# Performance work log

Hardware: AMD Instinct MI355X
Metric: run time of the kernel (lower is better)

## Reference

```python
import jax, jax.numpy as jnp
import numpy as np

NUM_HEADS = 16
D_KV = 64
NUM_BUCKETS = 32
MAX_DISTANCE = 128


def _relative_position_bucket(rel_pos, num_buckets=NUM_BUCKETS, max_distance=MAX_DISTANCE):
    # bidirectional bucketing (dec_or_not=False -> b_di=True in source)
    nb = num_buckets // 2
    buckets = (rel_pos > 0).astype(jnp.int32) * nb
    rel = jnp.abs(rel_pos)
    max_exact = nb // 2
    is_small = rel < max_exact
    # guard log(0); masked out by is_small anyway
    rel_if_large = max_exact + (
        jnp.log(jnp.maximum(rel, 1).astype(jnp.float32) / max_exact)
        / np.log(max_distance / max_exact) * (nb - max_exact)
    ).astype(jnp.int32)
    rel_if_large = jnp.minimum(rel_if_large, nb - 1)
    return buckets + jnp.where(is_small, rel, rel_if_large)


def setup_inputs() -> dict:
    key = jax.random.key(0)
    ks = jax.random.split(key, 6)
    B, S, D = 2, 2048, 1024
    s = 1.0 / np.sqrt(D)
    return {
        "hidden_states": jax.random.normal(ks[0], (B, S, D), jnp.float32),
        "Wq": jax.random.normal(ks[1], (D, NUM_HEADS * D_KV), jnp.float32) * s,
        "Wk": jax.random.normal(ks[2], (D, NUM_HEADS * D_KV), jnp.float32) * s,
        "Wv": jax.random.normal(ks[3], (D, NUM_HEADS * D_KV), jnp.float32) * s,
        "Wo": jax.random.normal(ks[4], (NUM_HEADS * D_KV, D), jnp.float32) * s,
        "rel_emb": jax.random.normal(ks[5], (NUM_BUCKETS, NUM_HEADS), jnp.float32),
    }


def reference(hidden_states, Wq, Wk, Wv, Wo, rel_emb):
    B, S, D = hidden_states.shape
    H, Dh = NUM_HEADS, D_KV

    def heads(x):  # [B,S,H*Dh] -> [B,H,S,Dh]
        return x.reshape(B, S, H, Dh).transpose(0, 2, 1, 3)

    q = heads(hidden_states @ Wq)
    k = heads(hidden_states @ Wk)
    v = heads(hidden_states @ Wv)

    # T5 attention: no 1/sqrt(d) scaling
    scores = jnp.einsum("bhqd,bhkd->bhqk", q, k)

    # relative position bias (bias_cal)
    pos = jnp.arange(S)
    rel_pos = pos[None, :] - pos[:, None]  # [S_q, S_k]
    buckets = _relative_position_bucket(rel_pos)
    bias = rel_emb[buckets]                       # [S,S,H]
    bias = bias.transpose(2, 0, 1)[None]          # [1,H,S,S]

    scores = scores + bias
    attn = jax.nn.softmax(scores.astype(jnp.float32), axis=-1).astype(scores.dtype)
    # dropout p=0 in eval -> identity
    out = jnp.einsum("bhqk,bhkd->bhqd", attn, v)
    out = out.transpose(0, 2, 1, 3).reshape(B, S, H * Dh)
    return out @ Wo
```

## Files before the change

kernel.cpp:

```cpp
#include <hip/hip_runtime.h>

typedef __bf16 bf16x8 __attribute__((ext_vector_type(8)));
typedef float f32x4 __attribute__((ext_vector_type(4)));

#define LDK 72
#define LOG2E 1.44269504088896f

__device__ __forceinline__ unsigned short bfbits(float x) {
  __bf16 h = (__bf16)x;
  return __builtin_bit_cast(unsigned short, h);
}

__device__ __forceinline__ void gload_lds16(const unsigned short* g, unsigned short* l) {
  __builtin_amdgcn_global_load_lds(
      (const __attribute__((address_space(1))) unsigned int*)(const void*)g,
      (__attribute__((address_space(3))) unsigned int*)(void*)l, 16, 0, 0);
}

__global__ void bias_table_kernel(const float* __restrict__ rel_emb,
                                  float* __restrict__ tab) {
  int i = blockIdx.x * 256 + threadIdx.x;
  int h = i >> 12;
  int idx = i & 4095;
  int rp = idx - 2048;
  int base = (rp > 0) ? 16 : 0;
  int rel = rp < 0 ? -rp : rp;
  int b;
  if (rel < 8) {
    b = rel;
  } else {
    b = 8 + (int)(log2f((float)rel * 0.125f) * 2.0f);
    if (b > 15) b = 15;
  }
  tab[h * 4096 + idx] = rel_emb[(base + b) * 16 + h] * LOG2E - 64.0f;
}

__global__ __launch_bounds__(256)
void hid_convert_kernel(const float* __restrict__ src, unsigned short* __restrict__ dst) {
  int idx = (blockIdx.x * 256 + threadIdx.x) * 8;
  float4 v0 = *(const float4*)(src + idx);
  float4 v1 = *(const float4*)(src + idx + 4);
  unsigned short o[8] = {bfbits(v0.x), bfbits(v0.y), bfbits(v0.z), bfbits(v0.w),
                         bfbits(v1.x), bfbits(v1.y), bfbits(v1.z), bfbits(v1.w)};
  *(uint4*)(dst + idx) = *(const uint4*)o;
}

__global__ __launch_bounds__(256)
void transpose_w_kernel(const float* __restrict__ W0, const float* __restrict__ W1,
                        const float* __restrict__ W2, const float* __restrict__ W3,
                        unsigned short* __restrict__ T0, unsigned short* __restrict__ T1,
                        unsigned short* __restrict__ T2, unsigned short* __restrict__ T3) {
  __shared__ __align__(16) unsigned short Tlds[64 * 68];
  const int mz = blockIdx.z;
  const float* W = mz == 0 ? W0 : (mz == 1 ? W1 : (mz == 2 ? W2 : W3));
  unsigned short* T = mz == 0 ? T0 : (mz == 1 ? T1 : (mz == 2 ? T2 : T3));
  const int k0 = blockIdx.y * 64, n0 = blockIdx.x * 64, tid = threadIdx.x;
#pragma unroll
  for (int p = 0; p < 4; ++p) {
    int idx = p * 256 + tid;
    int kk = idx >> 4, nc = idx & 15;
    float4 v = *(const float4*)(W + (size_t)(k0 + kk) * 1024 + n0 + nc * 4);
    ushort4 s;
    s.x = bfbits(v.x); s.y = bfbits(v.y); s.z = bfbits(v.z); s.w = bfbits(v.w);
    *(ushort4*)(Tlds + kk * 68 + nc * 4) = s;
  }
  __syncthreads();
#pragma unroll
  for (int p = 0; p < 2; ++p) {
    int idx = p * 256 + tid;
    int n = idx >> 3, c = idx & 7;
    unsigned short tmp[8];
#pragma unroll
    for (int j = 0; j < 8; ++j) tmp[j] = Tlds[(c * 8 + j) * 68 + n];
    *(uint4*)(T + (size_t)(n0 + n) * 1024 + k0 + c * 8) = *(const uint4*)tmp;
  }
}

template <bool OUT_F32, int BN>
__global__ __launch_bounds__(256)
void gemm_kernel(const unsigned short* __restrict__ A,
                 const unsigned short* __restrict__ Wt0,
                 const unsigned short* __restrict__ Wt1,
                 const unsigned short* __restrict__ Wt2,
                 void* __restrict__ O0v, void* __restrict__ O1v, void* __restrict__ O2v,
                 float scale0) {
  constexpr int NBLK = 1024 / BN;
  constexpr int NT = BN / 32;
  __shared__ __align__(16) unsigned short Alds[128 * 64];
  __shared__ __align__(16) unsigned short Wlds[BN * 64];
  const int tid = threadIdx.x;
  const int which = blockIdx.x / NBLK;
  const int n0 = (blockIdx.x % NBLK) * BN;
  const int m0 = blockIdx.y * 128;
  const unsigned short* Wt = which == 0 ? Wt0 : (which == 1 ? Wt1 : Wt2);
  void* Ov = which == 0 ? O0v : (which == 1 ? O1v : O2v);
  const int wave = tid >> 6, lane = tid & 63, quad = lane >> 4, col = lane & 15;
  const int wm = (wave >> 1) * 64, wn = (wave & 1) * (BN / 2);
  const int wbase = tid & ~63;
  const int sw = col & 7;

  f32x4 acc[4][NT] = {};

  for (int kt = 0; kt < 16; ++kt) {
    const int k0 = kt * 64;
    __syncthreads();
#pragma unroll
    for (int p = 0; p < 4; ++p) {
      int idx = p * 256 + tid;
      int m = idx >> 3, c = idx & 7;
      int cs = c ^ (m & 7);
      gload_lds16(A + (size_t)(m0 + m) * 1024 + k0 + cs * 8,
                  Alds + (size_t)(p * 256 + wbase) * 8);
    }
#pragma unroll
    for (int p = 0; p < BN / 32; ++p) {
      int idx = p * 256 + tid;
      int n = idx >> 3, c = idx & 7;
      int cs = c ^ (n & 7);
      gload_lds16(Wt + (size_t)(n0 + n) * 1024 + k0 + cs * 8,
                  Wlds + (size_t)(p * 256 + wbase) * 8);
    }
    __syncthreads();
#pragma unroll
    for (int ks = 0; ks < 2; ++ks) {
      bf16x8 af[4], wf[NT];
      const int j = ((ks * 4) ^ sw) ^ (sw & 3);
#pragma unroll
      for (int mt = 0; mt < 4; ++mt)
        af[mt] = *(const bf16x8*)(Alds + (wm + mt * 16 + col) * 64 +
                                  (((ks * 4 + quad) ^ sw) * 8));
#pragma unroll
      for (int nt = 0; nt < NT; ++nt)
        wf[nt] = *(const bf16x8*)(Wlds + (wn + nt * 16 + col) * 64 +
                                  (((ks * 4 + quad) ^ sw) * 8));
      (void)j;
#pragma unroll
      for (int mt = 0; mt < 4; ++mt)
#pragma unroll
        for (int nt = 0; nt < NT; ++nt)
          acc[mt][nt] = __builtin_amdgcn_mfma_f32_16x16x32_bf16(af[mt], wf[nt], acc[mt][nt], 0, 0, 0);
    }
  }
  if (!OUT_F32 && which == 2) {
    unsigned short* Ot = (unsigned short*)Ov;
#pragma unroll
    for (int nt = 0; nt < NT; ++nt)
#pragma unroll
      for (int mt = 0; mt < 4; ++mt) {
        int n = n0 + wn + nt * 16 + col;
        int m = m0 + wm + mt * 16 + quad * 4;
        ushort4 s;
        s.x = bfbits(acc[mt][nt][0]); s.y = bfbits(acc[mt][nt][1]);
        s.z = bfbits(acc[mt][nt][2]); s.w = bfbits(acc[mt][nt][3]);
        *(ushort4*)(Ot + (size_t)n * 4096 + m) = s;
      }
  } else {
    const float sc = (which == 0) ? scale0 : 1.0f;
#pragma unroll
    for (int mt = 0; mt < 4; ++mt)
#pragma unroll
      for (int nt = 0; nt < NT; ++nt)
#pragma unroll
        for (int r = 0; r < 4; ++r) {
          int m = m0 + wm + mt * 16 + quad * 4 + r;
          int n = n0 + wn + nt * 16 + col;
          float x = acc[mt][nt][r] * sc;
          if (OUT_F32)
            ((float*)Ov)[(size_t)m * 1024 + n] = x;
          else
            ((unsigned short*)Ov)[(size_t)m * 1024 + n] = bfbits(x);
        }
  }
}

__global__ __launch_bounds__(256)
void attn_kernel(unsigned short* __restrict__ q_ws,
                 const unsigned short* __restrict__ k_ws,
                 const unsigned short* __restrict__ vt_ws,
                 const float* __restrict__ bias_tab) {
  __shared__ __align__(16) unsigned short Klds[64 * 64];
  __shared__ __align__(16) unsigned short Vlds[64 * 64];
  __shared__ __align__(16) unsigned short Plds[128 * LDK];
  __shared__ float bias_lds[192];
  __shared__ float l_sh[128];
  const int tid = threadIdx.x;
  const int q0 = blockIdx.x * 128;
  const int bh = blockIdx.y;
  const int b = bh >> 4, h = bh & 15;
  const int wave = tid >> 6, lane = tid & 63, quad = lane >> 4, col = lane & 15;
  const int wbase = tid & ~63;
  const int sw = col & 7;

  bf16x8 qf[2][2];
#pragma unroll
  for (int nt = 0; nt < 2; ++nt) {
    size_t row = (size_t)(b * 2048 + q0 + wave * 32 + nt * 16 + col) * 1024 + h * 64;
    qf[nt][0] = *(const bf16x8*)(q_ws + row + quad * 8);
    qf[nt][1] = *(const bf16x8*)(q_ws + row + 32 + quad * 8);
  }
  const float bias_far_pos = bias_tab[h * 4096 + 2048 + 512];
  const float bias_far_neg = bias_tab[h * 4096 + 2048 - 512];

  float l_lane[2] = {0.f, 0.f};
  f32x4 of[2][4] = {};

  for (int kt = 0; kt < 32; ++kt) {
    const int k0 = kt * 64;
    const int diff = k0 - q0;
    const bool far = (diff >= 256) || (diff <= -192);
    __syncthreads();
#pragma unroll
    for (int p = 0; p < 2; ++p) {
      int idx = p * 256 + tid;
      int key = idx >> 3, c = idx & 7;
      int cs = c ^ (key & 7);
      gload_lds16(k_ws + (size_t)(b * 2048 + k0 + key) * 1024 + h * 64 + cs * 8,
                  Klds + (size_t)(p * 256 + wbase) * 8);
    }
#pragma unroll
    for (int p = 0; p < 2; ++p) {
      int idx = p * 256 + tid;
      int d = idx >> 3, c = idx & 7;
      int cs = c ^ (d & 7);
      gload_lds16(vt_ws + (size_t)(h * 64 + d) * 4096 + b * 2048 + k0 + cs * 8,
                  Vlds + (size_t)(p * 256 + wbase) * 8);
    }
    if (!far && tid < 191)
      bias_lds[tid] = bias_tab[h * 4096 + 2048 + k0 - q0 - 127 + tid];
    __syncthreads();

    f32x4 st[4][2];
    if (far) {
      const float c0 = (diff > 0) ? bias_far_pos : bias_far_neg;
#pragma unroll
      for (int mt = 0; mt < 4; ++mt)
#pragma unroll
        for (int nt = 0; nt < 2; ++nt)
#pragma unroll
          for (int r = 0; r < 4; ++r) st[mt][nt][r] = c0;
    } else {
#pragma unroll
      for (int mt = 0; mt < 4; ++mt)
#pragma unroll
        for (int nt = 0; nt < 2; ++nt)
#pragma unroll
          for (int r = 0; r < 4; ++r)
            st[mt][nt][r] =
                bias_lds[(mt * 16 + quad * 4 + r) - (wave * 32 + nt * 16 + col) + 127];
    }
#pragma unroll
    for (int ks = 0; ks < 2; ++ks)
#pragma unroll
      for (int mt = 0; mt < 4; ++mt) {
        bf16x8 kf = *(const bf16x8*)(Klds + (mt * 16 + col) * 64 +
                                     (((ks * 4 + quad) ^ sw) * 8));
        st[mt][0] = __builtin_amdgcn_mfma_f32_16x16x32_bf16(kf, qf[0][ks], st[mt][0], 0, 0, 0);
        st[mt][1] = __builtin_amdgcn_mfma_f32_16x16x32_bf16(kf, qf[1][ks], st[mt][1], 0, 0, 0);
      }

#pragma unroll
    for (int nt = 0; nt < 2; ++nt)
#pragma unroll
      for (int mt = 0; mt < 4; ++mt) {
        float p0 = __builtin_amdgcn_exp2f(st[mt][nt][0]);
        float p1 = __builtin_amdgcn_exp2f(st[mt][nt][1]);
        float p2 = __builtin_amdgcn_exp2f(st[mt][nt][2]);
        float p3 = __builtin_amdgcn_exp2f(st[mt][nt][3]);
        l_lane[nt] += (p0 + p1) + (p2 + p3);
        ushort4 pk;
        pk.x = bfbits(p0); pk.y = bfbits(p1); pk.z = bfbits(p2); pk.w = bfbits(p3);
        *(ushort4*)(Plds + (wave * 32 + nt * 16 + col) * LDK + mt * 16 + quad * 4) = pk;
      }
    __threadfence_block();

#pragma unroll
    for (int ks = 0; ks < 2; ++ks) {
      bf16x8 pf0 = *(const bf16x8*)(Plds + (wave * 32 + col) * LDK + ks * 32 + quad * 8);
      bf16x8 pf1 = *(const bf16x8*)(Plds + (wave * 32 + 16 + col) * LDK + ks * 32 + quad * 8);
#pragma unroll
      for (int dn = 0; dn < 4; ++dn) {
        bf16x8 vf = *(const bf16x8*)(Vlds + (dn * 16 + col) * 64 +
                                     (((ks * 4 + quad) ^ sw) * 8));
        of[0][dn] = __builtin_amdgcn_mfma_f32_16x16x32_bf16(pf0, vf, of[0][dn], 0, 0, 0);
        of[1][dn] = __builtin_amdgcn_mfma_f32_16x16x32_bf16(pf1, vf, of[1][dn], 0, 0, 0);
      }
    }
  }

#pragma unroll
  for (int nt = 0; nt < 2; ++nt) {
    l_lane[nt] += __shfl_xor(l_lane[nt], 16, 64);
    l_lane[nt] += __shfl_xor(l_lane[nt], 32, 64);
  }
  l_sh[wave * 32 + col] = l_lane[0];
  l_sh[wave * 32 + 16 + col] = l_lane[1];
  __syncthreads();
#pragma unroll
  for (int mtp = 0; mtp < 2; ++mtp)
#pragma unroll
    for (int r = 0; r < 4; ++r) {
      float inv = 1.0f / fmaxf(l_sh[wave * 32 + mtp * 16 + quad * 4 + r], 1e-30f);
      size_t row = (size_t)(b * 2048 + q0 + wave * 32 + mtp * 16 + quad * 4 + r);
#pragma unroll
      for (int dn = 0; dn < 4; ++dn)
        q_ws[row * 1024 + h * 64 + dn * 16 + col] = bfbits(of[mtp][dn][r] * inv);
    }
}

extern "C" void kernel_launch(void* const* d_in, const int* in_sizes, int n_in,
                              void* d_out, int out_size, void* d_ws, size_t ws_size,
                              hipStream_t stream) {
  const float* hidden = (const float*)d_in[0];
  const float* Wq = (const float*)d_in[1];
  const float* Wk = (const float*)d_in[2];
  const float* Wv = (const float*)d_in[3];
  const float* Wo = (const float*)d_in[4];
  const float* rel_emb = (const float*)d_in[5];
  float* out = (float*)d_out;

  unsigned short* q_ws = (unsigned short*)d_ws;
  unsigned short* k_ws = q_ws + 4194304;
  unsigned short* vt_ws = k_ws + 4194304;
  unsigned short* wt_q = vt_ws + 4194304;
  unsigned short* wt_k = wt_q + 1048576;
  unsigned short* wt_v = wt_k + 1048576;
  unsigned short* wt_o = wt_v + 1048576;
  float* bias_tab = (float*)(wt_o + 1048576);
  unsigned short* hid_bf = (unsigned short*)d_out;

  bias_table_kernel<<<256, 256, 0, stream>>>(rel_emb, bias_tab);
  hid_convert_kernel<<<2048, 256, 0, stream>>>(hidden, hid_bf);
  transpose_w_kernel<<<dim3(16, 16, 4), 256, 0, stream>>>(
      Wq, Wk, Wv, Wo, wt_q, wt_k, wt_v, wt_o);
  gemm_kernel<false, 128><<<dim3(24, 32), 256, 0, stream>>>(
      hid_bf, wt_q, wt_k, wt_v, q_ws, k_ws, vt_ws, LOG2E);
  attn_kernel<<<dim3(16, 32), 256, 0, stream>>>(q_ws, k_ws, vt_ws, bias_tab);
  gemm_kernel<true, 64><<<dim3(16, 32), 256, 0, stream>>>(
      q_ws, wt_o, wt_o, wt_o, out, out, out, 1.0f);
}
```

Baseline: 204.4 us.

## Double-buffer attention K/V/bias tiles and merge prelude kernels into one launch

The attention loop now keeps two LDS buffers for the K, V and bias tiles. It issues the asynchronous global-to-LDS loads for the next key tile right after the barrier, so they overlap the current tile's QK, exp and PV MFMA work, and one of the two barriers per iteration goes away. The bias-table, hidden-state conversion and weight-transpose kernels are merged into a single prelude launch that branches on block index, which removes two launch gaps. In exchange, LDS use per attention block roughly doubles for the K/V tiles, which could lower occupancy. The GEMM kernel also loses an unused variable.

```diff
diff --git a/kernel.cpp b/kernel.cpp
--- a/kernel.cpp
+++ b/kernel.cpp
@@ -17,62 +17,62 @@
       (__attribute__((address_space(3))) unsigned int*)(void*)l, 16, 0, 0);
 }
 
-__global__ void bias_table_kernel(const float* __restrict__ rel_emb,
-                                  float* __restrict__ tab) {
-  int i = blockIdx.x * 256 + threadIdx.x;
-  int h = i >> 12;
-  int idx = i & 4095;
-  int rp = idx - 2048;
-  int base = (rp > 0) ? 16 : 0;
-  int rel = rp < 0 ? -rp : rp;
-  int b;
-  if (rel < 8) {
-    b = rel;
+__global__ __launch_bounds__(256)
+void prelude_kernel(const float* __restrict__ hidden, unsigned short* __restrict__ hid_bf,
+                    const float* __restrict__ W0, const float* __restrict__ W1,
+                    const float* __restrict__ W2, const float* __restrict__ W3,
+                    unsigned short* __restrict__ T0, unsigned short* __restrict__ T1,
+                    unsigned short* __restrict__ T2, unsigned short* __restrict__ T3,
+                    const float* __restrict__ rel_emb, float* __restrict__ bias_tab) {
+  __shared__ __align__(16) unsigned short Tlds[64 * 68];
+  const int bx = blockIdx.x, tid = threadIdx.x;
+  if (bx < 2048) {
+    int idx = (bx * 256 + tid) * 8;
+    float4 v0 = *(const float4*)(hidden + idx);
+    float4 v1 = *(const float4*)(hidden + idx + 4);
+    unsigned short o[8] = {bfbits(v0.x), bfbits(v0.y), bfbits(v0.z), bfbits(v0.w),
+                           bfbits(v1.x), bfbits(v1.y), bfbits(v1.z), bfbits(v1.w)};
+    *(uint4*)(hid_bf + idx) = *(const uint4*)o;
+  } else if (bx < 3072) {
+    int flat = bx - 2048;
+    int mz = flat >> 8;
+    int k0 = ((flat >> 4) & 15) * 64, n0 = (flat & 15) * 64;
+    const float* W = mz == 0 ? W0 : (mz == 1 ? W1 : (mz == 2 ? W2 : W3));
+    unsigned short* T = mz == 0 ? T0 : (mz == 1 ? T1 : (mz == 2 ? T2 : T3));
+#pragma unroll
+    for (int p = 0; p < 4; ++p) {
+      int idx = p * 256 + tid;
+      int kk = idx >> 4, nc = idx & 15;
+      float4 v = *(const float4*)(W + (size_t)(k0 + kk) * 1024 + n0 + nc * 4);
+      ushort4 s;
+      s.x = bfbits(v.x); s.y = bfbits(v.y); s.z = bfbits(v.z); s.w = bfbits(v.w);
+      *(ushort4*)(Tlds + kk * 68 + nc * 4) = s;
+    }
+    __syncthreads();
+#pragma unroll
+    for (int p = 0; p < 2; ++p) {
+      int idx = p * 256 + tid;
+      int n = idx >> 3, c = idx & 7;
+      unsigned short tmp[8];
+#pragma unroll
+      for (int j = 0; j < 8; ++j) tmp[j] = Tlds[(c * 8 + j) * 68 + n];
+      *(uint4*)(T + (size_t)(n0 + n) * 1024 + k0 + c * 8) = *(const uint4*)tmp;
+    }
   } else {
-    b = 8 + (int)(log2f((float)rel * 0.125f) * 2.0f);
-    if (b > 15) b = 15;
-  }
-  tab[h * 4096 + idx] = rel_emb[(base + b) * 16 + h] * LOG2E - 64.0f;
-}
-
-__global__ __launch_bounds__(256)
-void hid_convert_kernel(const float* __restrict__ src, unsigned short* __restrict__ dst) {
-  int idx = (blockIdx.x * 256 + threadIdx.x) * 8;
-  float4 v0 = *(const float4*)(src + idx);
-  float4 v1 = *(const float4*)(src + idx + 4);
-  unsigned short o[8] = {bfbits(v0.x), bfbits(v0.y), bfbits(v0.z), bfbits(v0.w),
-                         bfbits(v1.x), bfbits(v1.y), bfbits(v1.z), bfbits(v1.w)};
-  *(uint4*)(dst + idx) = *(const uint4*)o;
-}
-
-__global__ __launch_bounds__(256)
-void transpose_w_kernel(const float* __restrict__ W0, const float* __restrict__ W1,
-                        const float* __restrict__ W2, const float* __restrict__ W3,
-                        unsigned short* __restrict__ T0, unsigned short* __restrict__ T1,
-                        unsigned short* __restrict__ T2, unsigned short* __restrict__ T3) {
-  __shared__ __align__(16) unsigned short Tlds[64 * 68];
-  const int mz = blockIdx.z;
-  const float* W = mz == 0 ? W0 : (mz == 1 ? W1 : (mz == 2 ? W2 : W3));
-  unsigned short* T = mz == 0 ? T0 : (mz == 1 ? T1 : (mz == 2 ? T2 : T3));
-  const int k0 = blockIdx.y * 64, n0 = blockIdx.x * 64, tid = threadIdx.x;
-#pragma unroll
-  for (int p = 0; p < 4; ++p) {
-    int idx = p * 256 + tid;
-    int kk = idx >> 4, nc = idx & 15;
-    float4 v = *(const float4*)(W + (size_t)(k0 + kk) * 1024 + n0 + nc * 4);
-    ushort4 s;
-    s.x = bfbits(v.x); s.y = bfbits(v.y); s.z = bfbits(v.z); s.w = bfbits(v.w);
-    *(ushort4*)(Tlds + kk * 68 + nc * 4) = s;
-  }
-  __syncthreads();
-#pragma unroll
-  for (int p = 0; p < 2; ++p) {
-    int idx = p * 256 + tid;
-    int n = idx >> 3, c = idx & 7;
-    unsigned short tmp[8];
-#pragma unroll
-    for (int j = 0; j < 8; ++j) tmp[j] = Tlds[(c * 8 + j) * 68 + n];
-    *(uint4*)(T + (size_t)(n0 + n) * 1024 + k0 + c * 8) = *(const uint4*)tmp;
+    int i = (bx - 3072) * 256 + tid;
+    int h = i >> 12;
+    int idx = i & 4095;
+    int rp = idx - 2048;
+    int base = (rp > 0) ? 16 : 0;
+    int rel = rp < 0 ? -rp : rp;
+    int b;
+    if (rel < 8) {
+      b = rel;
+    } else {
+      b = 8 + (int)(log2f((float)rel * 0.125f) * 2.0f);
+      if (b > 15) b = 15;
+    }
+    bias_tab[h * 4096 + idx] = rel_emb[(base + b) * 16 + h] * LOG2E - 64.0f;
   }
 }
 
@@ -124,7 +124,6 @@
 #pragma unroll
     for (int ks = 0; ks < 2; ++ks) {
       bf16x8 af[4], wf[NT];
-      const int j = ((ks * 4) ^ sw) ^ (sw & 3);
 #pragma unroll
       for (int mt = 0; mt < 4; ++mt)
         af[mt] = *(const bf16x8*)(Alds + (wm + mt * 16 + col) * 64 +
@@ -133,7 +132,6 @@
       for (int nt = 0; nt < NT; ++nt)
         wf[nt] = *(const bf16x8*)(Wlds + (wn + nt * 16 + col) * 64 +
                                   (((ks * 4 + quad) ^ sw) * 8));
-      (void)j;
 #pragma unroll
       for (int mt = 0; mt < 4; ++mt)
 #pragma unroll
@@ -178,10 +176,10 @@
                  const unsigned short* __restrict__ k_ws,
                  const unsigned short* __restrict__ vt_ws,
                  const float* __restrict__ bias_tab) {
-  __shared__ __align__(16) unsigned short Klds[64 * 64];
-  __shared__ __align__(16) unsigned short Vlds[64 * 64];
+  __shared__ __align__(16) unsigned short Klds[2][64 * 64];
+  __shared__ __align__(16) unsigned short Vlds[2][64 * 64];
   __shared__ __align__(16) unsigned short Plds[128 * LDK];
-  __shared__ float bias_lds[192];
+  __shared__ float bias_lds[2][192];
   __shared__ float l_sh[128];
   const int tid = threadIdx.x;
   const int q0 = blockIdx.x * 128;
@@ -204,30 +202,39 @@
   float l_lane[2] = {0.f, 0.f};
   f32x4 of[2][4] = {};
 
+  auto stage = [&](int kt, int buf) {
+    const int k0 = kt * 64;
+#pragma unroll
+    for (int p = 0; p < 2; ++p) {
+      int idx = p * 256 + tid;
+      int key = idx >> 3, c = idx & 7;
+      int cs = c ^ (key & 7);
+      gload_lds16(k_ws + (size_t)(b * 2048 + k0 + key) * 1024 + h * 64 + cs * 8,
+                  Klds[buf] + (size_t)(p * 256 + wbase) * 8);
+    }
+#pragma unroll
+    for (int p = 0; p < 2; ++p) {
+      int idx = p * 256 + tid;
+      int d = idx >> 3, c = idx & 7;
+      int cs = c ^ (d & 7);
+      gload_lds16(vt_ws + (size_t)(h * 64 + d) * 4096 + b * 2048 + k0 + cs * 8,
+                  Vlds[buf] + (size_t)(p * 256 + wbase) * 8);
+    }
+    const int diff = k0 - q0;
+    const bool farr = (diff >= 256) || (diff <= -192);
+    if (!farr && tid < 191)
+      bias_lds[buf][tid] = bias_tab[h * 4096 + 2048 + k0 - q0 - 127 + tid];
+  };
+
+  stage(0, 0);
+
   for (int kt = 0; kt < 32; ++kt) {
+    const int cur = kt & 1;
     const int k0 = kt * 64;
     const int diff = k0 - q0;
     const bool far = (diff >= 256) || (diff <= -192);
     __syncthreads();
-#pragma unroll
-    for (int p = 0; p < 2; ++p) {
-      int idx = p * 256 + tid;
-      int key = idx >> 3, c = idx & 7;
-      int cs = c ^ (key & 7);
-      gload_lds16(k_ws + (size_t)(b * 2048 + k0 + key) * 1024 + h * 64 + cs * 8,
-                  Klds + (size_t)(p * 256 + wbase) * 8);
-    }
-#pragma unroll
-    for (int p = 0; p < 2; ++p) {
-      int idx = p * 256 + tid;
-      int d = idx >> 3, c = idx & 7;
-      int cs = c ^ (d & 7);
-      gload_lds16(vt_ws + (size_t)(h * 64 + d) * 4096 + b * 2048 + k0 + cs * 8,
-                  Vlds + (size_t)(p * 256 + wbase) * 8);
-    }
-    if (!far && tid < 191)
-      bias_lds[tid] = bias_tab[h * 4096 + 2048 + k0 - q0 - 127 + tid];
-    __syncthreads();
+    if (kt + 1 < 32) stage(kt + 1, cur ^ 1);
 
     f32x4 st[4][2];
     if (far) {
@@ -246,13 +253,13 @@
 #pragma unroll
           for (int r = 0; r < 4; ++r)
             st[mt][nt][r] =
-                bias_lds[(mt * 16 + quad * 4 + r) - (wave * 32 + nt * 16 + col) + 127];
+                bias_lds[cur][(mt * 16 + quad * 4 + r) - (wave * 32 + nt * 16 + col) + 127];
     }
 #pragma unroll
     for (int ks = 0; ks < 2; ++ks)
 #pragma unroll
       for (int mt = 0; mt < 4; ++mt) {
-        bf16x8 kf = *(const bf16x8*)(Klds + (mt * 16 + col) * 64 +
+        bf16x8 kf = *(const bf16x8*)(Klds[cur] + (mt * 16 + col) * 64 +
                                      (((ks * 4 + quad) ^ sw) * 8));
         st[mt][0] = __builtin_amdgcn_mfma_f32_16x16x32_bf16(kf, qf[0][ks], st[mt][0], 0, 0, 0);
         st[mt][1] = __builtin_amdgcn_mfma_f32_16x16x32_bf16(kf, qf[1][ks], st[mt][1], 0, 0, 0);
@@ -279,7 +286,7 @@
       bf16x8 pf1 = *(const bf16x8*)(Plds + (wave * 32 + 16 + col) * LDK + ks * 32 + quad * 8);
 #pragma unroll
       for (int dn = 0; dn < 4; ++dn) {
-        bf16x8 vf = *(const bf16x8*)(Vlds + (dn * 16 + col) * 64 +
+        bf16x8 vf = *(const bf16x8*)(Vlds[cur] + (dn * 16 + col) * 64 +
                                      (((ks * 4 + quad) ^ sw) * 8));
         of[0][dn] = __builtin_amdgcn_mfma_f32_16x16x32_bf16(pf0, vf, of[0][dn], 0, 0, 0);
         of[1][dn] = __builtin_amdgcn_mfma_f32_16x16x32_bf16(pf1, vf, of[1][dn], 0, 0, 0);
@@ -328,10 +335,8 @@
   float* bias_tab = (float*)(wt_o + 1048576);
   unsigned short* hid_bf = (unsigned short*)d_out;
 
-  bias_table_kernel<<<256, 256, 0, stream>>>(rel_emb, bias_tab);
-  hid_convert_kernel<<<2048, 256, 0, stream>>>(hidden, hid_bf);
-  transpose_w_kernel<<<dim3(16, 16, 4), 256, 0, stream>>>(
-      Wq, Wk, Wv, Wo, wt_q, wt_k, wt_v, wt_o);
+  prelude_kernel<<<3328, 256, 0, stream>>>(hidden, hid_bf, Wq, Wk, Wv, Wo,
+                                           wt_q, wt_k, wt_v, wt_o, rel_emb, bias_tab);
   gemm_kernel<false, 128><<<dim3(24, 32), 256, 0, stream>>>(
       hid_bf, wt_q, wt_k, wt_v, q_ws, k_ws, vt_ws, LOG2E);
   attn_kernel<<<dim3(16, 32), 256, 0, stream>>>(q_ws, k_ws, vt_ws, bias_tab);
```

After: 196.8 us. -3.7%, faster.
